# Optimization experiments

Hardware: AMD Instinct MI355X
Metric: run time of the kernel (lower is better)

The kernel has to match this reference:

```python
import jax, jax.numpy as jnp
import numpy as np

N = 20000      # atoms
E = 240000     # edges (avg degree ~12, matches _AVG_DEGREE_MATPES)
C = 128        # sphere_channels
ZMAX = 100     # max_num_elements
NG = 600       # GaussianSmearing(0, cutoff, 600, 2.0)
CUTOFF = 6.0
WIDTH = 2.0    # basis_width_scalar
RESCALE = 12.0 # _AVG_DEGREE_MATPES
LN_EPS = 1e-5
# xyz -> (y,z,x): real-SH component order for l=1, so Wigner D^(1) = P R P^T
P = np.array([[0.,1.,0.],[0.,0.,1.],[1.,0.,0.]], dtype=np.float32)


def _layernorm(x, g, b):
    mu = jnp.mean(x, axis=-1, keepdims=True)
    var = jnp.mean((x - mu) ** 2, axis=-1, keepdims=True)
    return g * (x - mu) * jax.lax.rsqrt(var + LN_EPS) + b


def init_edge_rot_mat(ev):
    # faithful port of init_edge_rot_mat (torch uses .detach())
    ev = jax.lax.stop_gradient(ev)
    dist = jnp.maximum(jnp.linalg.norm(ev, axis=1, keepdims=True), 1e-8)
    nx = ev / dist
    ref = jnp.eye(3, dtype=ev.dtype)[jnp.argmin(jnp.abs(nx), axis=1)]
    nz = jnp.cross(nx, ref)
    nz = nz / jnp.maximum(jnp.linalg.norm(nz, axis=1, keepdims=True), 1e-8)
    ny = jnp.cross(nx, nz)
    ny = ny / jnp.maximum(jnp.linalg.norm(ny, axis=1, keepdims=True), 1e-8)
    # edge_rot_mat_inv has columns [nz, nx, -ny]; rot = inv^T -> rows [nz, nx, -ny]
    return jnp.stack([nz, nx, -ny], axis=1)  # [E,3,3]


def setup_inputs() -> dict:
    key = jax.random.key(0)
    ks = jax.random.split(key, 10)
    s = 0.02
    return {
        'edge_distance_vec': jax.random.normal(ks[0], (E, 3), jnp.float32) * 2.0,
        'sphere_emb': jax.random.normal(ks[1], (ZMAX, C), jnp.float32) * s,
        'src_emb': jax.random.normal(ks[2], (ZMAX, C), jnp.float32) * s,
        'tgt_emb': jax.random.normal(ks[3], (ZMAX, C), jnp.float32) * s,
        'W1': jax.random.normal(ks[4], (NG + 2 * C, C), jnp.float32) * s,
        'b1': jnp.zeros((C,), jnp.float32),
        'g1': jnp.ones((C,), jnp.float32),
        'be1': jnp.zeros((C,), jnp.float32),
        'W2': jax.random.normal(ks[5], (C, C), jnp.float32) * s,
        'b2': jnp.zeros((C,), jnp.float32),
        'g2': jnp.ones((C,), jnp.float32),
        'be2': jnp.zeros((C,), jnp.float32),
        'W3': jax.random.normal(ks[6], (C, 2 * C), jnp.float32) * s,
        'b3': jnp.zeros((2 * C,), jnp.float32),
        'atomic_numbers': jax.random.randint(ks[7], (N,), 0, ZMAX),
        'edge_index': jax.random.randint(ks[8], (2, E), 0, N),
    }


def reference(edge_distance_vec, sphere_emb, src_emb, tgt_emb,
              W1, b1, g1, be1, W2, b2, g2, be2, W3, b3,
              atomic_numbers, edge_index):
    src, dst = edge_index[0], edge_index[1]
    Pm = jnp.asarray(P)
    # per-edge rotation to edge-aligned frame and its l=1 Wigner matrix
    rot = init_edge_rot_mat(edge_distance_vec)               # [E,3,3]
    D1 = jnp.einsum('ij,ejk,lk->eil', Pm, rot, Pm)           # [E,3,3]
    # Gaussian distance expansion (600 basis fns)
    dist = jnp.linalg.norm(edge_distance_vec, axis=1)        # [E]
    offsets = jnp.linspace(0.0, CUTOFF, NG)
    coeff = -0.5 / (WIDTH * (offsets[1] - offsets[0])) ** 2
    gauss = jnp.exp(coeff * (dist[:, None] - offsets[None, :]) ** 2)  # [E,600]
    # edge features: distance basis + source/target atom embeddings
    x_edge = jnp.concatenate(
        [gauss, src_emb[atomic_numbers[src]], tgt_emb[atomic_numbers[dst]]], axis=1)
    # RadialFunction: Linear->LN->SiLU x2, final Linear -> m=0 coefficients
    h = jax.nn.silu(_layernorm(x_edge @ W1 + b1, g1, be1))
    h = jax.nn.silu(_layernorm(h @ W2 + b2, g2, be2))
    m0 = (h @ W3 + b3).reshape(E, 2, C)   # (l=0,m=0) and (l=1,m=0)
    # rotate back to global frame: blockdiag(1, D1)^T applied to (m0[0]; 0, m0[1], 0)
    l0 = m0[:, 0][:, None, :]                                 # [E,1,C]
    l1 = jnp.einsum('ei,ec->eic', D1[:, 1, :], m0[:, 1])      # (D1^T v)_i with v=(0,a,0)
    msg = jnp.concatenate([l0, l1], axis=1)                   # [E,4,C]
    # scatter-sum messages to target nodes, rescale by avg degree
    x_deg = jnp.zeros((N, 4, C), msg.dtype).at[dst].add(msg) / RESCALE
    # node init: atom embedding into l=0 slot, plus edge-degree embedding
    x = x_deg.at[:, 0].add(sphere_emb[atomic_numbers])
    return x
```

## Files before the change

kernel.cpp:

```cpp
#include <hip/hip_runtime.h>
#include <stdint.h>

#define EE 240000
#define NN 20000
#define NB 4096

typedef __attribute__((ext_vector_type(4))) float f32x4;
typedef __attribute__((ext_vector_type(8))) __bf16 bf16x8;
typedef __attribute__((ext_vector_type(8))) short s16x8;

union V8 { s16x8 s; bf16x8 b; uint4 u; };

static constexpr double DD_ = 6.0 / 599.0;
static constexpr double L2E_ = 1.4426950408889634;
static constexpr float GC2 = (float)((-0.5 / (4.0 * DD_ * DD_)) * L2E_);
static constexpr float RC0  = (float)((-0.5 / 4.0) * L2E_);
static constexpr float RLIN = (float)(2.0 * (-0.5 / (4.0 * DD_ * DD_)) * L2E_ * DD_);
static constexpr float QC   = (float)0.7788007830714049;

__device__ __forceinline__ float b2f(unsigned short u) {
    return __uint_as_float(((unsigned)u) << 16);
}
__device__ __forceinline__ unsigned short f2b(float f) {
    unsigned u = __float_as_uint(f);
    return (unsigned short)((u + 0x7fffu + ((u >> 16) & 1u)) >> 16);
}
__device__ __forceinline__ unsigned cvtpk(float lo, float hi) {
    unsigned r;
    asm("v_cvt_pk_bf16_f32 %0, %1, %2" : "=v"(r) : "v"(lo), "v"(hi));
    return r;
}
__device__ __forceinline__ unsigned short ldc(const void* p, int i, bool isb) {
    return isb ? ((const unsigned short*)p)[i] : f2b(((const float*)p)[i]);
}
__device__ __forceinline__ float ldf(const void* p, int i, bool isb) {
    return isb ? b2f(((const unsigned short*)p)[i]) : ((const float*)p)[i];
}
__device__ __forceinline__ bool probe_isb(const void* g1) {
    return ((const unsigned*)g1)[0] != 0x3F800000u;
}

__device__ __forceinline__ int kperm(int p) {
    int wi = p >> 1;
    return ((wi >> 4) << 5) + (wi & 15) + ((p & 1) << 4);
}

#define PREP_PARAMS_TOTAL (77824 + 16384 + 32768 + 25600 + 25600 + 1024)
#define PB ((PREP_PARAMS_TOTAL + 255) / 256)
#define EB ((EE + 255) / 256)

__global__ void prep_all(const void* ev, const int* __restrict__ an,
                         const int* __restrict__ ei,
                         const void* W1, const void* W2, const void* W3,
                         const void* se, const void* te,
                         const void* b1, const void* g1, const void* be1,
                         const void* b2, const void* g2, const void* be2,
                         const void* b3,
                         unsigned short* __restrict__ W1T,
                         unsigned short* __restrict__ W2T,
                         unsigned short* __restrict__ W3T,
                         float2* __restrict__ SEWT,
                         float2* __restrict__ TEWT,
                         unsigned short* __restrict__ vecs,
                         uint4* __restrict__ sedge_u, float4* __restrict__ d1_out,
                         int* __restrict__ deg, int* __restrict__ bhist) {
    bool isb = probe_isb(g1);
    int bid = blockIdx.x;
    if (bid < PB) {
        int t = bid * 256 + threadIdx.x;
        if (t < 77824) {
            int j = t & 7, n = (t >> 3) & 127, kb = t >> 10;
            int k = kb * 8 + j;
            W1T[t] = (k < 600) ? ldc(W1, k * 128 + n, isb) : (unsigned short)0;
            return;
        }
        t -= 77824;
        if (t < 16384) {
            int j = t & 7, n = (t >> 3) & 127, kb = t >> 10;
            W2T[t] = ldc(W2, kperm(kb * 8 + j) * 128 + n, isb);
            return;
        }
        t -= 16384;
        if (t < 32768) {
            int j = t & 7, n = (t >> 3) & 255, kb = t >> 11;
            W3T[t] = ldc(W3, kperm(kb * 8 + j) * 256 + n, isb);
            return;
        }
        t -= 32768;
        if (t < 25600) {
            int word = t >> 2, sub = t & 3;
            int z = word >> 6, wi = word & 63;
            int c0 = ((wi >> 4) << 5) | (wi & 15), c1 = c0 + 16;
            float a0 = 0.f, a1 = 0.f;
            int k0 = sub * 32;
            for (int k = k0; k < k0 + 32; ++k) {
                float sv = ldf(se, z * 128 + k, isb);
                a0 += sv * ldf(W1, (600 + k) * 128 + c0, isb);
                a1 += sv * ldf(W1, (600 + k) * 128 + c1, isb);
            }
            a0 += __shfl_xor(a0, 1); a0 += __shfl_xor(a0, 2);
            a1 += __shfl_xor(a1, 1); a1 += __shfl_xor(a1, 2);
            if (sub == 0) {
                float2 w;
                w.x = a0 + ldf(b1, c0, isb);
                w.y = a1 + ldf(b1, c1, isb);
                SEWT[word] = w;
            }
            return;
        }
        t -= 25600;
        if (t < 25600) {
            int word = t >> 2, sub = t & 3;
            int z = word >> 6, wi = word & 63;
            int c0 = ((wi >> 4) << 5) | (wi & 15), c1 = c0 + 16;
            float a0 = 0.f, a1 = 0.f;
            int k0 = sub * 32;
            for (int k = k0; k < k0 + 32; ++k) {
                float tv = ldf(te, z * 128 + k, isb);
                a0 += tv * ldf(W1, (728 + k) * 128 + c0, isb);
                a1 += tv * ldf(W1, (728 + k) * 128 + c1, isb);
            }
            a0 += __shfl_xor(a0, 1); a0 += __shfl_xor(a0, 2);
            a1 += __shfl_xor(a1, 1); a1 += __shfl_xor(a1, 2);
            if (sub == 0) {
                float2 w; w.x = a0; w.y = a1;
                TEWT[word] = w;
            }
            return;
        }
        t -= 25600;
        if (t < 128) { vecs[t] = ldc(b1, t, isb); return; }
        t -= 128;
        if (t < 128) { vecs[128 + t] = ldc(g1, t, isb); return; }
        t -= 128;
        if (t < 128) { vecs[256 + t] = ldc(be1, t, isb); return; }
        t -= 128;
        if (t < 128) { vecs[384 + t] = ldc(b2, t, isb); return; }
        t -= 128;
        if (t < 128) { vecs[512 + t] = ldc(g2, t, isb); return; }
        t -= 128;
        if (t < 128) { vecs[640 + t] = ldc(be2, t, isb); return; }
        t -= 128;
        if (t < 256) { vecs[768 + t] = ldc(b3, t, isb); return; }
        return;
    }
    int e = (bid - PB) * 256 + threadIdx.x;
    if (e >= EE) return;
    float x = ldf(ev, e * 3 + 0, isb);
    float y = ldf(ev, e * 3 + 1, isb);
    float z = ldf(ev, e * 3 + 2, isb);
    float nrm = sqrtf(x * x + y * y + z * z);
    float rn = __builtin_amdgcn_rcpf(fmaxf(nrm, 1e-8f));
    float nx0 = x * rn, nx1 = y * rn, nx2 = z * rn;
    float a0 = fabsf(nx0), a1 = fabsf(nx1), a2 = fabsf(nx2);
    int idx = 0; float mv = a0;
    if (a1 < mv) { idx = 1; mv = a1; }
    if (a2 < mv) { idx = 2; }
    float r0 = (idx == 0) ? 1.f : 0.f;
    float r1 = (idx == 1) ? 1.f : 0.f;
    float r2 = (idx == 2) ? 1.f : 0.f;
    float z0 = nx1 * r2 - nx2 * r1;
    float z1 = nx2 * r0 - nx0 * r2;
    float z2 = nx0 * r1 - nx1 * r0;
    float rz = rsqrtf(fmaxf(z0 * z0 + z1 * z1 + z2 * z2, 1e-16f));
    z0 *= rz; z1 *= rz; z2 *= rz;
    float y0 = nx1 * z2 - nx2 * z1;
    float y1 = nx2 * z0 - nx0 * z2;
    float y2 = nx0 * z1 - nx1 * z0;
    float ry = rsqrtf(fmaxf(y0 * y0 + y1 * y1 + y2 * y2, 1e-16f));
    y0 *= ry; y1 *= ry; y2 *= ry;
    float4 dv; dv.x = -y1; dv.y = -y2; dv.z = -y0; dv.w = 0.f;
    d1_out[e] = dv;
    int zsv = an[ei[e]];
    int dst = ei[EE + e];
    int zdv = an[dst];
    uint4 su;
    su.x = __float_as_uint(nrm);
    su.y = (unsigned)zsv | ((unsigned)zdv << 16);
    su.z = (unsigned)e;
    su.w = 0;
    sedge_u[e] = su;
    atomicAdd(&deg[dst], 1);
    int b = min(NB - 1, (int)(nrm * 512.0f));
    atomicAdd(&bhist[b], 1);
}

__global__ __launch_bounds__(1024) void scan_all(
    const int* __restrict__ deg, const int* __restrict__ bhist,
    int* __restrict__ row_start, int* __restrict__ cursor, int* __restrict__ bcursor) {
    __shared__ int lds[17];
    int t = threadIdx.x;
    int lane = t & 63, wid = t >> 6;
    int base = t * 20;
    int loc[20]; int ls = 0;
#pragma unroll
    for (int j = 0; j < 20; ++j) {
        int i = base + j;
        ls += (i < NN) ? deg[i] : 0;
        loc[j] = ls;
    }
    int x = ls;
#pragma unroll
    for (int s = 1; s < 64; s <<= 1) { int v = __shfl_up(x, s); if (lane >= s) x += v; }
    if (lane == 63) lds[wid] = x;
    __syncthreads();
    if (wid == 0) {
        int w = (lane < 16) ? lds[lane] : 0;
#pragma unroll
        for (int s = 1; s < 16; s <<= 1) { int v = __shfl_up(w, s); if (lane >= s) w += v; }
        if (lane < 16) lds[lane] = w;
    }
    __syncthreads();
    int off = (wid ? lds[wid - 1] : 0) + x - ls;
#pragma unroll
    for (int j = 0; j < 20; ++j) {
        int i = base + j;
        if (i < NN) {
            row_start[i + 1] = off + loc[j];
            cursor[i] = off + (j ? loc[j - 1] : 0);
        }
    }
    if (t == 0) row_start[0] = 0;
    __syncthreads();
    int b4 = t * 4;
    int l4[4]; int bs = 0;
#pragma unroll
    for (int j = 0; j < 4; ++j) { bs += bhist[b4 + j]; l4[j] = bs; }
    x = bs;
#pragma unroll
    for (int s = 1; s < 64; s <<= 1) { int v = __shfl_up(x, s); if (lane >= s) x += v; }
    if (lane == 63) lds[wid] = x;
    __syncthreads();
    if (wid == 0) {
        int w = (lane < 16) ? lds[lane] : 0;
#pragma unroll
        for (int s = 1; s < 16; s <<= 1) { int v = __shfl_up(w, s); if (lane >= s) w += v; }
        if (lane < 16) lds[lane] = w;
    }
    __syncthreads();
    int boff = (wid ? lds[wid - 1] : 0) + x - bs;
#pragma unroll
    for (int j = 0; j < 4; ++j) bcursor[b4 + j] = boff + (j ? l4[j - 1] : 0);
}

__global__ void fill_sorted(const int* __restrict__ ei,
                            const uint4* __restrict__ sedge_u,
                            const float4* __restrict__ d1v,
                            int* __restrict__ cursor, int* __restrict__ bcursor,
                            uint4* __restrict__ sedge_s, float4* __restrict__ d1s) {
    int e = blockIdx.x * 256 + threadIdx.x;
    if (e >= EE) return;
    uint4 su = sedge_u[e];
    int dst = ei[EE + e];
    int p = atomicAdd(&cursor[dst], 1);
    float d = __uint_as_float(su.x);
    int b = min(NB - 1, (int)(d * 512.0f));
    int sp = atomicAdd(&bcursor[b], 1);
    su.z = (unsigned)p;
    sedge_s[sp] = su;
    d1s[p] = d1v[e];
}

__device__ __forceinline__ void ln_silu(f32x4 (&acc)[2][8],
                                        const unsigned short* __restrict__ gamma,
                                        const unsigned short* __restrict__ beta,
                                        int i16, int quad,
                                        unsigned short (*ht)[136]) {
    float gm[8], bt[8];
#pragma unroll
    for (int nt = 0; nt < 8; ++nt) {
        gm[nt] = b2f(gamma[nt * 16 + i16]);
        bt[nt] = b2f(beta[nt * 16 + i16]);
    }
#pragma unroll
    for (int mt = 0; mt < 2; ++mt) {
#pragma unroll
        for (int r = 0; r < 4; ++r) {
            float s = 0.f, s2 = 0.f;
#pragma unroll
            for (int nt = 0; nt < 8; ++nt) {
                float v = acc[mt][nt][r];
                s += v; s2 += v * v;
            }
#pragma unroll
            for (int m = 1; m < 16; m <<= 1) {
                s += __shfl_xor(s, m);
                s2 += __shfl_xor(s2, m);
            }
            float mu = s * (1.f / 128.f);
            float var = s2 * (1.f / 128.f) - mu * mu;
            float rs = rsqrtf(var + 1e-5f);
            unsigned* wrow = (unsigned*)ht[mt * 16 + quad * 4 + r];
#pragma unroll
            for (int ntp = 0; ntp < 4; ++ntp) {
                float zz[2];
#pragma unroll
                for (int h = 0; h < 2; ++h) {
                    int nt = 2 * ntp + h;
                    float y = gm[nt] * (acc[mt][nt][r] - mu) * rs + bt[nt];
                    zz[h] = y * __builtin_amdgcn_rcpf(1.f + exp2f(-1.4426950409f * y));
                }
                wrow[ntp * 16 + i16] = cvtpk(zz[0], zz[1]);
            }
        }
    }
}

template <bool MSG>
__global__ __launch_bounds__(256, 4) void edge_mlp(
    const unsigned short* __restrict__ W1T, const unsigned short* __restrict__ W2T,
    const unsigned short* __restrict__ W3T,
    const float2* __restrict__ SEWT, const float2* __restrict__ TEWT,
    const unsigned short* __restrict__ vecs,
    const uint4* __restrict__ sedge,
    const int* __restrict__ ei, const float4* __restrict__ d1v,
    unsigned* __restrict__ msg, float* __restrict__ xacc) {
    __shared__ __align__(16) unsigned short htile_s[4][32][136];
    int tid = threadIdx.x;
    int wave = tid >> 6, lane = tid & 63;
    int i16 = lane & 15, quad = lane >> 4;
    unsigned short (*ht)[136] = htile_s[wave];
    int mbase = blockIdx.x * 128 + wave * 32;

    uint4 s0 = sedge[mbase + i16];
    uint4 s1 = sedge[mbase + 16 + i16];
    float dd0 = __uint_as_float(s0.x), dd1 = __uint_as_float(s1.x);
    int dpz0 = (int)s0.z, dpz1 = (int)s1.z;

    float dmn = fminf(dd0, dd1), dmx = fmaxf(dd0, dd1);
#pragma unroll
    for (int m = 1; m < 64; m <<= 1) {
        dmn = fminf(dmn, __shfl_xor(dmn, m));
        dmx = fmaxf(dmx, __shfl_xor(dmx, m));
    }
    int klo = (int)floorf((dmn - 0.285f) * (599.0f / 6.0f));
    int khi = (int)ceilf((dmx + 0.285f) * (599.0f / 6.0f));
    int ka = min(max(klo, 0) >> 5, 19);
    int kb = min((min(khi, 607) >> 5) + 1, 19);

    f32x4 acc[2][8];
#pragma unroll
    for (int mt = 0; mt < 2; ++mt) {
        unsigned sy = mt ? s1.y : s0.y;
#pragma unroll
        for (int r = 0; r < 4; ++r) {
            unsigned zy = (unsigned)__shfl((int)sy, quad * 4 + r);
            const float2* sw = SEWT + (zy & 0xFFFFu) * 64 + i16;
            const float2* tw = TEWT + (zy >> 16) * 64 + i16;
#pragma unroll
            for (int ntp = 0; ntp < 4; ++ntp) {
                float2 a = sw[ntp * 16];
                float2 b = tw[ntp * 16];
                acc[mt][2 * ntp][r]     = a.x + b.x;
                acc[mt][2 * ntp + 1][r] = a.y + b.y;
            }
        }
    }

#pragma unroll 1
    for (int ks = ka; ks < kb; ++ks) {
        int k0 = ks * 32 + quad * 8;
        V8 af[2];
#pragma unroll
        for (int mt = 0; mt < 2; ++mt) {
            float dm = mt ? dd1 : dd0;
            float t0 = dm - (float)k0 * (float)(6.0 / 599.0);
            float e0 = exp2f(GC2 * t0 * t0);
            float r = exp2f(fmaf(-RLIN, t0, RC0));
            float e1 = e0 * r; r *= QC;
            float e2 = e1 * r; r *= QC;
            float e3 = e2 * r; r *= QC;
            float e4 = e3 * r; r *= QC;
            float e5 = e4 * r; r *= QC;
            float e6 = e5 * r; r *= QC;
            float e7 = e6 * r;
            af[mt].u.x = cvtpk(e0, e1);
            af[mt].u.y = cvtpk(e2, e3);
            af[mt].u.z = cvtpk(e4, e5);
            af[mt].u.w = cvtpk(e6, e7);
        }
        const unsigned short* w1p = W1T + (((ks * 4 + quad) * 128 + i16) << 3);
#pragma unroll
        for (int nt = 0; nt < 8; ++nt) {
            V8 bf_; bf_.s = *(const s16x8*)(w1p + nt * 128);
            acc[0][nt] = __builtin_amdgcn_mfma_f32_16x16x32_bf16(af[0].b, bf_.b, acc[0][nt], 0, 0, 0);
            acc[1][nt] = __builtin_amdgcn_mfma_f32_16x16x32_bf16(af[1].b, bf_.b, acc[1][nt], 0, 0, 0);
        }
    }
    ln_silu(acc, vecs + 128, vecs + 256, i16, quad, ht);

#pragma unroll
    for (int mt = 0; mt < 2; ++mt)
#pragma unroll
        for (int nt = 0; nt < 8; ++nt) {
            float b = b2f(vecs[384 + nt * 16 + i16]);
#pragma unroll
            for (int q = 0; q < 4; ++q) acc[mt][nt][q] = b;
        }
#pragma unroll 1
    for (int ks = 0; ks < 4; ++ks) {
        int k0 = ks * 32 + quad * 8;
        V8 a0, a1;
        a0.s = *(const s16x8*)&ht[i16][k0];
        a1.s = *(const s16x8*)&ht[16 + i16][k0];
        const unsigned short* w2p = W2T + (((ks * 4 + quad) * 128 + i16) << 3);
#pragma unroll
        for (int nt = 0; nt < 8; ++nt) {
            V8 bf_; bf_.s = *(const s16x8*)(w2p + nt * 128);
            acc[0][nt] = __builtin_amdgcn_mfma_f32_16x16x32_bf16(a0.b, bf_.b, acc[0][nt], 0, 0, 0);
            acc[1][nt] = __builtin_amdgcn_mfma_f32_16x16x32_bf16(a1.b, bf_.b, acc[1][nt], 0, 0, 0);
        }
    }
    ln_silu(acc, vecs + 512, vecs + 640, i16, quad, ht);

#pragma unroll 1
    for (int half = 0; half < 2; ++half) {
#pragma unroll
        for (int mt = 0; mt < 2; ++mt)
#pragma unroll
            for (int nt = 0; nt < 8; ++nt) {
                float b = b2f(vecs[768 + half * 128 + nt * 16 + i16]);
#pragma unroll
                for (int q = 0; q < 4; ++q) acc[mt][nt][q] = b;
            }
#pragma unroll 1
        for (int ks = 0; ks < 4; ++ks) {
            int k0 = ks * 32 + quad * 8;
            V8 a0, a1;
            a0.s = *(const s16x8*)&ht[i16][k0];
            a1.s = *(const s16x8*)&ht[16 + i16][k0];
            const unsigned short* w3p = W3T + (((ks * 4 + quad) * 256 + half * 128 + i16) << 3);
#pragma unroll
            for (int nt = 0; nt < 8; ++nt) {
                V8 bf_; bf_.s = *(const s16x8*)(w3p + nt * 128);
                acc[0][nt] = __builtin_amdgcn_mfma_f32_16x16x32_bf16(a0.b, bf_.b, acc[0][nt], 0, 0, 0);
                acc[1][nt] = __builtin_amdgcn_mfma_f32_16x16x32_bf16(a1.b, bf_.b, acc[1][nt], 0, 0, 0);
            }
        }
        if constexpr (MSG) {
#pragma unroll
            for (int mt = 0; mt < 2; ++mt) {
                int dpz = mt ? dpz1 : dpz0;
#pragma unroll
                for (int r = 0; r < 4; ++r) {
                    int dp = __shfl(dpz, quad * 4 + r);
                    uint4 v;
                    v.x = cvtpk(acc[mt][0][r], acc[mt][1][r]);
                    v.y = cvtpk(acc[mt][2][r], acc[mt][3][r]);
                    v.z = cvtpk(acc[mt][4][r], acc[mt][5][r]);
                    v.w = cvtpk(acc[mt][6][r], acc[mt][7][r]);
                    *(uint4*)(msg + (size_t)dp * 128 + half * 64 + i16 * 4) = v;
                }
            }
        } else {
#pragma unroll
            for (int mt = 0; mt < 2; ++mt) {
#pragma unroll
                for (int r = 0; r < 4; ++r) {
                    int eidx = mbase + mt * 16 + quad * 4 + r;
                    int dn = ei[EE + eidx];
                    float* xb = xacc + (size_t)dn * 512;
                    if (half == 0) {
#pragma unroll
                        for (int nt = 0; nt < 8; ++nt)
                            atomicAdd(xb + nt * 16 + i16, acc[mt][nt][r]);
                    } else {
                        float4 dv = d1v[eidx];
#pragma unroll
                        for (int nt = 0; nt < 8; ++nt) {
                            float val = acc[mt][nt][r];
                            atomicAdd(xb + 128 + nt * 16 + i16, val * dv.x);
                            atomicAdd(xb + 256 + nt * 16 + i16, val * dv.y);
                            atomicAdd(xb + 384 + nt * 16 + i16, val * dv.z);
                        }
                    }
                }
            }
        }
    }
}

__global__ __launch_bounds__(256) void gather(
    const unsigned* __restrict__ msg,
    const float4* __restrict__ d1s, const int* __restrict__ row_start,
    const void* __restrict__ sp, const void* __restrict__ g1,
    const int* __restrict__ an, float* __restrict__ out) {
    __shared__ float cbuf[2][8][64];
    int tid = threadIdx.x;
    int w = tid >> 6, l = tid & 63;
    int nl = w >> 1, sub = w & 1;
    int n = blockIdx.x * 2 + nl;
    int cl = (l & 3) * 32 + (l >> 2);
    int i0 = row_start[n], i1 = row_start[n + 1];
    float a0 = 0.f, a1 = 0.f, x0 = 0.f, x1 = 0.f,
          y0 = 0.f, y1 = 0.f, z0 = 0.f, z1 = 0.f;
#pragma unroll 4
    for (int i = i0 + sub; i < i1; i += 2) {
        unsigned m0 = msg[(size_t)i * 128 + l];
        unsigned m1 = msg[(size_t)i * 128 + 64 + l];
        float4 dv = d1s[i];
        float p0 = b2f((unsigned short)m0), p1 = b2f((unsigned short)(m0 >> 16));
        float q0 = b2f((unsigned short)m1), q1 = b2f((unsigned short)(m1 >> 16));
        a0 += p0; a1 += p1;
        x0 += q0 * dv.x; x1 += q1 * dv.x;
        y0 += q0 * dv.y; y1 += q1 * dv.y;
        z0 += q0 * dv.z; z1 += q1 * dv.z;
    }
    if (sub) {
        cbuf[nl][0][l] = a0; cbuf[nl][1][l] = a1;
        cbuf[nl][2][l] = x0; cbuf[nl][3][l] = x1;
        cbuf[nl][4][l] = y0; cbuf[nl][5][l] = y1;
        cbuf[nl][6][l] = z0; cbuf[nl][7][l] = z1;
    }
    __syncthreads();
    if (!sub) {
        a0 += cbuf[nl][0][l]; a1 += cbuf[nl][1][l];
        x0 += cbuf[nl][2][l]; x1 += cbuf[nl][3][l];
        y0 += cbuf[nl][4][l]; y1 += cbuf[nl][5][l];
        z0 += cbuf[nl][6][l]; z1 += cbuf[nl][7][l];
        bool isb = probe_isb(g1);
        float* ob = out + (size_t)n * 512;
        int zb = an[n] * 128 + cl;
        constexpr float R = 1.f / 12.f;
        ob[cl]            = a0 * R + ldf(sp, zb, isb);
        ob[cl + 16]       = a1 * R + ldf(sp, zb + 16, isb);
        ob[128 + cl]      = x0 * R;
        ob[128 + cl + 16] = x1 * R;
        ob[256 + cl]      = y0 * R;
        ob[256 + cl + 16] = y1 * R;
        ob[384 + cl]      = z0 * R;
        ob[384 + cl + 16] = z1 * R;
    }
}

__global__ void finalize(const float* __restrict__ xacc, const void* __restrict__ sp,
                         const void* __restrict__ g1,
                         const int* __restrict__ an, float* __restrict__ out) {
    int t = blockIdx.x * 256 + threadIdx.x;
    bool isb = probe_isb(g1);
    int n = t >> 9, sc = t & 511;
    float v = xacc[t] * (1.f / 12.f);
    if (sc < 128) v += ldf(sp, an[n] * 128 + sc, isb);
    out[t] = v;
}

extern "C" void kernel_launch(void* const* d_in, const int* in_sizes, int n_in,
                              void* d_out, int out_size, void* d_ws, size_t ws_size,
                              hipStream_t stream) {
    const void* ev         = d_in[0];
    const void* sphere_emb = d_in[1];
    const void* src_emb    = d_in[2];
    const void* tgt_emb    = d_in[3];
    const void* W1  = d_in[4];  const void* b1  = d_in[5];
    const void* g1  = d_in[6];  const void* be1 = d_in[7];
    const void* W2  = d_in[8];  const void* b2  = d_in[9];
    const void* g2  = d_in[10]; const void* be2 = d_in[11];
    const void* W3  = d_in[12]; const void* b3  = d_in[13];
    const int* an   = (const int*)d_in[14];
    const int* ei   = (const int*)d_in[15];

    char* ws = (char*)d_ws;
    const size_t NEED_MSG = 132000000;

    if (ws_size >= NEED_MSG) {
        size_t off = 0;
        unsigned* msg = (unsigned*)(ws + off); off += (size_t)EE * 512;
        uint4* sedge_u = (uint4*)(ws + 0);
        float4* d1v    = (float4*)(ws + 3840000);
        float4* d1s    = (float4*)(ws + off);  off += (size_t)EE * 16;
        uint4* sedge_s = (uint4*)(ws + off);   off += (size_t)EE * 16;
        int* deg       = (int*)(ws + off);     off += (size_t)NN * 4;
        int* bhist     = (int*)(ws + off);     off += NB * 4;
        int* row_start = (int*)(ws + off);     off += (size_t)(NN + 4) * 4;
        int* cursor    = (int*)(ws + off);     off += (size_t)NN * 4;
        int* bcursor   = (int*)(ws + off);     off += NB * 4;
        unsigned short* W1T = (unsigned short*)(ws + off); off += 77824 * 2;
        unsigned short* W2T = (unsigned short*)(ws + off); off += 128 * 128 * 2;
        unsigned short* W3T = (unsigned short*)(ws + off); off += 256 * 128 * 2;
        float2* SEWT   = (float2*)(ws + off);  off += 6400 * 8;
        float2* TEWT   = (float2*)(ws + off);  off += 6400 * 8;
        unsigned short* vecs = (unsigned short*)(ws + off); off += 1024 * 2;

        hipMemsetAsync(deg, 0, (size_t)(NN + NB) * 4, stream);
        prep_all<<<PB + EB, 256, 0, stream>>>(
            ev, an, ei, W1, W2, W3, src_emb, tgt_emb,
            b1, g1, be1, b2, g2, be2, b3,
            W1T, W2T, W3T, SEWT, TEWT, vecs, sedge_u, d1v, deg, bhist);
        scan_all<<<1, 1024, 0, stream>>>(deg, bhist, row_start, cursor, bcursor);
        fill_sorted<<<(EE + 255) / 256, 256, 0, stream>>>(
            ei, sedge_u, d1v, cursor, bcursor, sedge_s, d1s);
        edge_mlp<true><<<EE / 128, 256, 0, stream>>>(
            W1T, W2T, W3T, SEWT, TEWT, vecs, sedge_s,
            (const int*)nullptr, (const float4*)nullptr, msg, (float*)nullptr);
        gather<<<NN / 2, 256, 0, stream>>>(msg, d1s, row_start,
                                           sphere_emb, g1, an, (float*)d_out);
    } else {
        size_t off = 0;
        float* xacc    = (float*)(ws + off);   off += (size_t)NN * 512 * 4;
        uint4* sedge_u = (uint4*)(ws + off);   off += (size_t)EE * 16;
        float4* d1v    = (float4*)(ws + off);  off += (size_t)EE * 16;
        int* deg       = (int*)(ws + off);     off += (size_t)NN * 4;
        int* bhist     = (int*)(ws + off);     off += NB * 4;
        unsigned short* W1T = (unsigned short*)(ws + off); off += 77824 * 2;
        unsigned short* W2T = (unsigned short*)(ws + off); off += 128 * 128 * 2;
        unsigned short* W3T = (unsigned short*)(ws + off); off += 256 * 128 * 2;
        float2* SEWT   = (float2*)(ws + off);  off += 6400 * 8;
        float2* TEWT   = (float2*)(ws + off);  off += 6400 * 8;
        unsigned short* vecs = (unsigned short*)(ws + off); off += 1024 * 2;

        hipMemsetAsync(xacc, 0, (size_t)NN * 512 * 4, stream);
        hipMemsetAsync(deg, 0, (size_t)(NN + NB) * 4, stream);
        prep_all<<<PB + EB, 256, 0, stream>>>(
            ev, an, ei, W1, W2, W3, src_emb, tgt_emb,
            b1, g1, be1, b2, g2, be2, b3,
            W1T, W2T, W3T, SEWT, TEWT, vecs, sedge_u, d1v, deg, bhist);
        edge_mlp<false><<<EE / 128, 256, 0, stream>>>(
            W1T, W2T, W3T, SEWT, TEWT, vecs, sedge_u, ei, d1v,
            (unsigned*)nullptr, xacc);
        finalize<<<(NN * 512) / 256, 256, 0, stream>>>(xacc, sphere_emb, g1, an,
                                                       (float*)d_out);
    }
}
```

Measured before the change: 314.7 us.

## Fuse scan and sorted fill into one cooperative kernel; widen gather loads

Replaces the single-block scan kernel and the separate fill kernel with one cooperative kernel. It does a multi-block scan of degrees and the distance histogram, then scatters edges into sorted order, using grid syncs between phases. It falls back to the old pair of kernels if the cooperative launch fails. The gather kernel now gives each wave one node and reads each message row with 16-byte loads, using half-wave row pairing and a shuffle reduction instead of a shared-memory combine. The grid sync adds its own overhead, and grid co-residency of 938 blocks is required for the cooperative path.

```diff
diff --git a/kernel.cpp b/kernel.cpp
--- a/kernel.cpp
+++ b/kernel.cpp
@@ -1,5 +1,8 @@
 #include <hip/hip_runtime.h>
+#include <hip/hip_cooperative_groups.h>
 #include <stdint.h>
+
+namespace cg = cooperative_groups;
 
 #define EE 240000
 #define NN 20000
@@ -185,6 +188,92 @@
     atomicAdd(&bhist[b], 1);
 }
 
+__global__ __launch_bounds__(256) void scan_fill(
+    const int* __restrict__ deg, const int* __restrict__ bhist,
+    const int* __restrict__ ei,
+    const uint4* __restrict__ sedge_u, const float4* __restrict__ d1v,
+    int* __restrict__ row_start, int* __restrict__ cursor,
+    int* __restrict__ bcursor, int* __restrict__ btot,
+    uint4* __restrict__ sedge_s, float4* __restrict__ d1s) {
+    cg::grid_group grid = cg::this_grid();
+    int bid = blockIdx.x, t = threadIdx.x;
+    int lane = t & 63, wv = t >> 6;
+    __shared__ int wsum[4];
+    if (bid < 79) {
+        int i = bid * 256 + t;
+        int v = (i < NN) ? deg[i] : 0;
+        int x = v;
+#pragma unroll
+        for (int s = 1; s < 64; s <<= 1) { int u = __shfl_up(x, s); if (lane >= s) x += u; }
+        if (lane == 63) wsum[wv] = x;
+        __syncthreads();
+        int pre = 0;
+        for (int w2 = 0; w2 < wv; ++w2) pre += wsum[w2];
+        x += pre;
+        if (i < NN) row_start[i + 1] = x;
+        if (t == 255) btot[bid] = x;
+    } else if (bid < 95) {
+        int j = (bid - 79) * 256 + t;
+        int v = bhist[j];
+        int x = v;
+#pragma unroll
+        for (int s = 1; s < 64; s <<= 1) { int u = __shfl_up(x, s); if (lane >= s) x += u; }
+        if (lane == 63) wsum[wv] = x;
+        __syncthreads();
+        int pre = 0;
+        for (int w2 = 0; w2 < wv; ++w2) pre += wsum[w2];
+        x += pre;
+        bcursor[j] = x;
+        if (t == 255) btot[bid] = x;
+    }
+    grid.sync();
+    if (bid == 0 && wv == 0) {
+        int carry = 0;
+        for (int base = 0; base < 79; base += 64) {
+            int idx = base + lane;
+            int v = (idx < 79) ? btot[idx] : 0;
+            int x = v;
+#pragma unroll
+            for (int s = 1; s < 64; s <<= 1) { int u = __shfl_up(x, s); if (lane >= s) x += u; }
+            if (idx < 79) btot[idx] = carry + x - v;
+            carry += __shfl(x, 63);
+        }
+    } else if (bid == 0 && wv == 1) {
+        int v = (lane < 16) ? btot[79 + lane] : 0;
+        int x = v;
+#pragma unroll
+        for (int s = 1; s < 16; s <<= 1) { int u = __shfl_up(x, s); if (lane >= s) x += u; }
+        if (lane < 16) btot[79 + lane] = x - v;
+    }
+    grid.sync();
+    if (bid < 79) {
+        int i = bid * 256 + t;
+        if (i < NN) {
+            int off = btot[bid];
+            int incl = row_start[i + 1] + off;
+            row_start[i + 1] = incl;
+            cursor[i] = incl - deg[i];
+        }
+        if (bid == 0 && t == 0) row_start[0] = 0;
+    } else if (bid < 95) {
+        int j = (bid - 79) * 256 + t;
+        bcursor[j] = bcursor[j] + btot[bid] - bhist[j];
+    }
+    grid.sync();
+    int e = bid * 256 + t;
+    if (e < EE) {
+        uint4 su = sedge_u[e];
+        int dst = ei[EE + e];
+        int p = atomicAdd(&cursor[dst], 1);
+        float d = __uint_as_float(su.x);
+        int b = min(NB - 1, (int)(d * 512.0f));
+        int sp2 = atomicAdd(&bcursor[b], 1);
+        su.z = (unsigned)p;
+        sedge_s[sp2] = su;
+        d1s[p] = d1v[e];
+    }
+}
+
 __global__ __launch_bounds__(1024) void scan_all(
     const int* __restrict__ deg, const int* __restrict__ bhist,
     int* __restrict__ row_start, int* __restrict__ cursor, int* __restrict__ bcursor) {
@@ -481,55 +570,72 @@
 }
 
 __global__ __launch_bounds__(256) void gather(
-    const unsigned* __restrict__ msg,
+    const uint4* __restrict__ msg4,
     const float4* __restrict__ d1s, const int* __restrict__ row_start,
     const void* __restrict__ sp, const void* __restrict__ g1,
     const int* __restrict__ an, float* __restrict__ out) {
-    __shared__ float cbuf[2][8][64];
     int tid = threadIdx.x;
-    int w = tid >> 6, l = tid & 63;
-    int nl = w >> 1, sub = w & 1;
-    int n = blockIdx.x * 2 + nl;
-    int cl = (l & 3) * 32 + (l >> 2);
+    int wv = tid >> 6, l = tid & 63;
+    int n = blockIdx.x * 4 + wv;
+    int i16 = l & 15;
+    bool o1lane = (l >> 4) & 1;
+    int rofs = l >> 5;
     int i0 = row_start[n], i1 = row_start[n + 1];
-    float a0 = 0.f, a1 = 0.f, x0 = 0.f, x1 = 0.f,
-          y0 = 0.f, y1 = 0.f, z0 = 0.f, z1 = 0.f;
-#pragma unroll 4
-    for (int i = i0 + sub; i < i1; i += 2) {
-        unsigned m0 = msg[(size_t)i * 128 + l];
-        unsigned m1 = msg[(size_t)i * 128 + 64 + l];
-        float4 dv = d1s[i];
-        float p0 = b2f((unsigned short)m0), p1 = b2f((unsigned short)(m0 >> 16));
-        float q0 = b2f((unsigned short)m1), q1 = b2f((unsigned short)(m1 >> 16));
-        a0 += p0; a1 += p1;
-        x0 += q0 * dv.x; x1 += q1 * dv.x;
-        y0 += q0 * dv.y; y1 += q1 * dv.y;
-        z0 += q0 * dv.z; z1 += q1 * dv.z;
-    }
-    if (sub) {
-        cbuf[nl][0][l] = a0; cbuf[nl][1][l] = a1;
-        cbuf[nl][2][l] = x0; cbuf[nl][3][l] = x1;
-        cbuf[nl][4][l] = y0; cbuf[nl][5][l] = y1;
-        cbuf[nl][6][l] = z0; cbuf[nl][7][l] = z1;
-    }
-    __syncthreads();
-    if (!sub) {
-        a0 += cbuf[nl][0][l]; a1 += cbuf[nl][1][l];
-        x0 += cbuf[nl][2][l]; x1 += cbuf[nl][3][l];
-        y0 += cbuf[nl][4][l]; y1 += cbuf[nl][5][l];
-        z0 += cbuf[nl][6][l]; z1 += cbuf[nl][7][l];
+    float a[8];
+    float xx[8], yy[8], zz[8];
+#pragma unroll
+    for (int k = 0; k < 8; ++k) { a[k] = 0.f; xx[k] = 0.f; yy[k] = 0.f; zz[k] = 0.f; }
+#pragma unroll 2
+    for (int r = i0; r < i1; r += 2) {
+        int row = r + rofs;
+        bool valid = row < i1;
+        uint4 v = msg4[(size_t)r * 32 + l];
+        float4 dv; dv.x = 0.f; dv.y = 0.f; dv.z = 0.f; dv.w = 0.f;
+        if (o1lane) dv = d1s[min(row, i1 - 1)];
+        float w0 = b2f((unsigned short)v.x), w1 = b2f((unsigned short)(v.x >> 16));
+        float w2 = b2f((unsigned short)v.y), w3 = b2f((unsigned short)(v.y >> 16));
+        float w4 = b2f((unsigned short)v.z), w5 = b2f((unsigned short)(v.z >> 16));
+        float w6 = b2f((unsigned short)v.w), w7 = b2f((unsigned short)(v.w >> 16));
+        if (valid) {
+            if (!o1lane) {
+                a[0] += w0; a[1] += w1; a[2] += w2; a[3] += w3;
+                a[4] += w4; a[5] += w5; a[6] += w6; a[7] += w7;
+            } else {
+                xx[0] += w0 * dv.x; xx[1] += w1 * dv.x; xx[2] += w2 * dv.x; xx[3] += w3 * dv.x;
+                xx[4] += w4 * dv.x; xx[5] += w5 * dv.x; xx[6] += w6 * dv.x; xx[7] += w7 * dv.x;
+                yy[0] += w0 * dv.y; yy[1] += w1 * dv.y; yy[2] += w2 * dv.y; yy[3] += w3 * dv.y;
+                yy[4] += w4 * dv.y; yy[5] += w5 * dv.y; yy[6] += w6 * dv.y; yy[7] += w7 * dv.y;
+                zz[0] += w0 * dv.z; zz[1] += w1 * dv.z; zz[2] += w2 * dv.z; zz[3] += w3 * dv.z;
+                zz[4] += w4 * dv.z; zz[5] += w5 * dv.z; zz[6] += w6 * dv.z; zz[7] += w7 * dv.z;
+            }
+        }
+    }
+#pragma unroll
+    for (int k = 0; k < 8; ++k) {
+        a[k]  += __shfl_xor(a[k], 32);
+        xx[k] += __shfl_xor(xx[k], 32);
+        yy[k] += __shfl_xor(yy[k], 32);
+        zz[k] += __shfl_xor(zz[k], 32);
+    }
+    constexpr float R = 1.f / 12.f;
+    float* ob = out + (size_t)n * 512;
+    if (l < 16) {
         bool isb = probe_isb(g1);
-        float* ob = out + (size_t)n * 512;
-        int zb = an[n] * 128 + cl;
-        constexpr float R = 1.f / 12.f;
-        ob[cl]            = a0 * R + ldf(sp, zb, isb);
-        ob[cl + 16]       = a1 * R + ldf(sp, zb + 16, isb);
-        ob[128 + cl]      = x0 * R;
-        ob[128 + cl + 16] = x1 * R;
-        ob[256 + cl]      = y0 * R;
-        ob[256 + cl + 16] = y1 * R;
-        ob[384 + cl]      = z0 * R;
-        ob[384 + cl + 16] = z1 * R;
+        int zb = an[n] * 128;
+#pragma unroll
+        for (int k = 0; k < 4; ++k) {
+            int c = k * 32 + i16;
+            ob[c]      = a[2 * k]     * R + ldf(sp, zb + c, isb);
+            ob[c + 16] = a[2 * k + 1] * R + ldf(sp, zb + c + 16, isb);
+        }
+    } else if (l < 32) {
+#pragma unroll
+        for (int k = 0; k < 4; ++k) {
+            int c = k * 32 + i16;
+            ob[128 + c]      = xx[2 * k] * R;      ob[128 + c + 16] = xx[2 * k + 1] * R;
+            ob[256 + c]      = yy[2 * k] * R;      ob[256 + c + 16] = yy[2 * k + 1] * R;
+            ob[384 + c]      = zz[2 * k] * R;      ob[384 + c + 16] = zz[2 * k + 1] * R;
+        }
     }
 }
 
@@ -574,6 +680,7 @@
         int* row_start = (int*)(ws + off);     off += (size_t)(NN + 4) * 4;
         int* cursor    = (int*)(ws + off);     off += (size_t)NN * 4;
         int* bcursor   = (int*)(ws + off);     off += NB * 4;
+        int* btot      = (int*)(ws + off);     off += 128 * 4;
         unsigned short* W1T = (unsigned short*)(ws + off); off += 77824 * 2;
         unsigned short* W2T = (unsigned short*)(ws + off); off += 128 * 128 * 2;
         unsigned short* W3T = (unsigned short*)(ws + off); off += 256 * 128 * 2;
@@ -586,13 +693,25 @@
             ev, an, ei, W1, W2, W3, src_emb, tgt_emb,
             b1, g1, be1, b2, g2, be2, b3,
             W1T, W2T, W3T, SEWT, TEWT, vecs, sedge_u, d1v, deg, bhist);
-        scan_all<<<1, 1024, 0, stream>>>(deg, bhist, row_start, cursor, bcursor);
-        fill_sorted<<<(EE + 255) / 256, 256, 0, stream>>>(
-            ei, sedge_u, d1v, cursor, bcursor, sedge_s, d1s);
+        {
+            const int* degc = deg; const int* bhistc = bhist;
+            const uint4* seuc = sedge_u; const float4* d1vc = d1v;
+            void* cargs[] = {(void*)&degc, (void*)&bhistc, (void*)&ei,
+                             (void*)&seuc, (void*)&d1vc,
+                             (void*)&row_start, (void*)&cursor, (void*)&bcursor,
+                             (void*)&btot, (void*)&sedge_s, (void*)&d1s};
+            hipError_t ce = hipLaunchCooperativeKernel(
+                (const void*)scan_fill, dim3(938), dim3(256), cargs, 0, stream);
+            if (ce != hipSuccess) {
+                scan_all<<<1, 1024, 0, stream>>>(deg, bhist, row_start, cursor, bcursor);
+                fill_sorted<<<(EE + 255) / 256, 256, 0, stream>>>(
+                    ei, sedge_u, d1v, cursor, bcursor, sedge_s, d1s);
+            }
+        }
         edge_mlp<true><<<EE / 128, 256, 0, stream>>>(
             W1T, W2T, W3T, SEWT, TEWT, vecs, sedge_s,
             (const int*)nullptr, (const float4*)nullptr, msg, (float*)nullptr);
-        gather<<<NN / 2, 256, 0, stream>>>(msg, d1s, row_start,
+        gather<<<NN / 4, 256, 0, stream>>>((const uint4*)msg, d1s, row_start,
                                            sphere_emb, g1, an, (float*)d_out);
     } else {
         size_t off = 0;
```

Result: slower. 628.0 us (+99.6%).
